# Optimization experiments

Measured on AMD Instinct MI355X. Metric: run time of the kernel, lower is better.

## Reference

```python
import jax, jax.numpy as jnp
import numpy as np

N_ATOMS = 25000
N_PAIRS = 500000
N_PROP = 16
C = 64          # channel width of pp/pi/ii/out layers
N_BASIS = 4     # radial basis functions per pair
DEPTH = 4       # number of GC blocks


def setup_inputs() -> dict:
    key = jax.random.key(0)
    ks = jax.random.split(key, 16)

    def w(k, shape):
        fan_in = shape[-2]
        return jax.random.normal(k, shape, jnp.float32) / jnp.sqrt(jnp.float32(fan_in))

    return {
        "ind_2": jax.random.randint(ks[0], (N_PAIRS, 2), 0, N_ATOMS),
        "prop": jax.random.normal(ks[1], (N_ATOMS, N_PROP), jnp.float32),
        "basis": jax.random.uniform(ks[2], (N_PAIRS, N_BASIS), jnp.float32),
        "pp0_w1": w(ks[3], (N_PROP, C)),
        "pp0_b1": jnp.zeros((C,), jnp.float32),
        "pp_w1": w(ks[4], (DEPTH - 1, C, C)),
        "pp_b1": jnp.zeros((DEPTH - 1, C), jnp.float32),
        "pp_w2": w(ks[5], (DEPTH, C, C)),
        "pp_b2": jnp.zeros((DEPTH, C), jnp.float32),
        "pi_w1": w(ks[6], (DEPTH, 2 * C, C)),
        "pi_b1": jnp.zeros((DEPTH, C), jnp.float32),
        "pi_w2": w(ks[7], (DEPTH, C, C * N_BASIS)),
        "pi_b2": jnp.zeros((DEPTH, C * N_BASIS), jnp.float32),
        "ii_w1": w(ks[8], (DEPTH, C, C)),
        "ii_w2": w(ks[9], (DEPTH, C, C)),
        "res0_w": w(ks[10], (N_PROP, C)),
        "out_w1": w(ks[11], (DEPTH, C, C)),
        "out_b1": jnp.zeros((DEPTH, C), jnp.float32),
        "out_w2": w(ks[12], (DEPTH, C, C)),
        "out_b2": jnp.zeros((DEPTH, C), jnp.float32),
        "out_wo": w(ks[13], (DEPTH, C, 1)),
    }


def _pinet_forward(ind_2, prop, basis,
                   pp0_w1, pp0_b1, pp_w1, pp_b1, pp_w2, pp_b2,
                   pi_w1, pi_b1, pi_w2, pi_b2,
                   ii_w1, ii_w2, res0_w,
                   out_w1, out_b1, out_w2, out_b2, out_wo):
    act = jnp.tanh
    n_atoms = prop.shape[0]
    n_basis = basis.shape[-1]
    c = pi_w2.shape[-1] // n_basis  # pi output channels
    depth = pp_w2.shape[0]
    ind_i = ind_2[:, 0]
    ind_j = ind_2[:, 1]

    p = prop
    output = jnp.zeros((n_atoms, out_wo.shape[-1]), p.dtype)
    for d in range(depth):
        # PPLayer (FFLayer with bias)
        if d == 0:
            h = act(p @ pp0_w1 + pp0_b1)
        else:
            h = act(p @ pp_w1[d - 1] + pp_b1[d - 1])
        h = act(h @ pp_w2[d] + pp_b2[d])
        # PILayer: gather pair endpoints, concat, FFLayer, basis contraction
        pij = jnp.concatenate([h[ind_i], h[ind_j]], axis=-1)  # (P, 2C)
        ww = act(pij @ pi_w1[d] + pi_b1[d])                   # (P, C)
        ww = act(ww @ pi_w2[d] + pi_b2[d])                    # (P, C*B)
        ww = ww.reshape(-1, c, n_basis)                       # (P, C, B)
        inter = jnp.einsum('pcb,pb->pc', ww, basis)           # (P, C)
        # IILayer (FFLayer, no bias)
        inter = act(inter @ ii_w1[d])
        inter = act(inter @ ii_w2[d])
        # IPLayer: scatter-sum pairs back to atoms
        newp = jax.ops.segment_sum(inter, ind_i, num_segments=n_atoms)
        # ResUpdate: linear projection if dims differ (block 0), else plain sum
        p = (p @ res0_w + newp) if d == 0 else (p + newp)
        # OutLayer: FFLayer + biasless linear, accumulated over depth
        o = act(p @ out_w1[d] + out_b1[d])
        o = act(o @ out_w2[d] + out_b2[d])
        output = output + o @ out_wo[d]
    return output


def reference(ind_2, prop, basis,
              pp0_w1, pp0_b1, pp_w1, pp_b1, pp_w2, pp_b2,
              pi_w1, pi_b1, pi_w2, pi_b2,
              ii_w1, ii_w2, res0_w,
              out_w1, out_b1, out_w2, out_b2, out_wo):
    return _pinet_forward(ind_2, prop, basis,
                          pp0_w1, pp0_b1, pp_w1, pp_b1, pp_w2, pp_b2,
                          pi_w1, pi_b1, pi_w2, pi_b2,
                          ii_w1, ii_w2, res0_w,
                          out_w1, out_b1, out_w2, out_b2, out_wo)
```

## Files before the change

kernel.cpp:

```cpp
#include <hip/hip_runtime.h>
#include <hip/hip_bf16.h>

#define N_ATOMS 25000
#define N_PAIRS 500000
#define DEPTH 4

typedef _Float16 f16x8 __attribute__((ext_vector_type(8)));
typedef float f32x16 __attribute__((ext_vector_type(16)));
typedef unsigned short u16;

__device__ __forceinline__ float tanh_fast(float x) {
    float e = __expf(2.0f * x);
    return 1.0f - 2.0f * __builtin_amdgcn_rcpf(e + 1.0f);
}

__device__ __forceinline__ void split_h(float x, u16& hi, u16& lo) {
    _Float16 h = (_Float16)x;
    _Float16 l = (_Float16)(x - (float)h);
    hi = *(u16*)&h;
    lo = *(u16*)&l;
}

__device__ __forceinline__ int swz8(int u) { return u ^ ((u >> 5) & 7); }

__global__ __launch_bounds__(256)
void prep_kernel(const float* __restrict__ piW1, const float* __restrict__ piW2,
                 const float* __restrict__ iiW1, const float* __restrict__ iiW2,
                 u16* __restrict__ img1, u16* __restrict__ img2, u16* __restrict__ imgab) {
    int gid = blockIdx.x * 256 + threadIdx.x;
    int d = gid >> 15, e = gid & 32767;
    u16 hi, lo;
    if (e < 8192) {
        int k = e >> 6, n = e & 63;
        split_h(piW1[d * 8192 + e], hi, lo);
        int ntw = n >> 5, colb = n & 31;
        int ks = k >> 4, lh = (k >> 3) & 1, j = k & 7;
        int off = ((ntw * 8 + ks) * 64 + lh * 32 + colb) * 8 + j;
        img1[d * 16384 + 0 * 8192 + off] = hi;
        img1[d * 16384 + 1 * 8192 + off] = lo;
    } else if (e < 24576) {
        int s = e - 8192;
        int k = s >> 8, n = s & 255;
        split_h(piW2[d * 16384 + s], hi, lo);
        int ch = n >> 2, t = n & 3;
        int ntw = ch >> 5, colb = ch & 31;
        int ks = k >> 4, lh = (k >> 3) & 1, j = k & 7;
        int off = (((ntw * 4 + t) * 4 + ks) * 64 + lh * 32 + colb) * 8 + j;
        img2[d * 32768 + 0 * 16384 + off] = hi;
        img2[d * 32768 + 1 * 16384 + off] = lo;
    } else {
        int stage = (e < 28672) ? 0 : 1;
        int s = e - (stage ? 28672 : 24576);
        int k = s >> 6, n = s & 63;
        float x = stage ? iiW2[d * 4096 + s] : iiW1[d * 4096 + s];
        split_h(x, hi, lo);
        int ntw = n >> 5, colb = n & 31;
        int ks = k >> 4, lh = (k >> 3) & 1, j = k & 7;
        int off = ((ntw * 4 + ks) * 64 + lh * 32 + colb) * 8 + j;
        imgab[d * 16384 + (stage * 2 + 0) * 4096 + off] = hi;
        imgab[d * 16384 + (stage * 2 + 1) * 4096 + off] = lo;
    }
}

__global__ __launch_bounds__(256)
void prep_b2(const float* __restrict__ piB2, float* __restrict__ b2p) {
    int d = blockIdx.x, n = threadIdx.x;
    int ch = n >> 2, t = n & 3;
    int np = (ch >> 5) * 128 + t * 32 + (ch & 31);
    b2p[d * 256 + np] = piB2[d * 256 + n];
}

template <int K, bool IS_D0>
__global__ __launch_bounds__(256)
void atom_mlp(const float* __restrict__ p_in,
              const float* __restrict__ W1, const float* __restrict__ b1,
              const float* __restrict__ W2, const float* __restrict__ b2,
              const float* __restrict__ res0_w,
              _Float16* __restrict__ h_hi, _Float16* __restrict__ h_lo,
              float* __restrict__ acc_out) {
    __shared__ float sP[4][64];
    __shared__ float sH[4][64];
    int tid = threadIdx.x;
    int al = tid >> 6, c = tid & 63;
    int a = blockIdx.x * 4 + al;
    if (c < K) sP[al][c] = p_in[a * K + c];
    __syncthreads();
    float s = b1[c];
#pragma unroll
    for (int k = 0; k < K; ++k) s += sP[al][k] * W1[k * 64 + c];
    float t1 = tanh_fast(s);
    float r;
    if (IS_D0) {
        r = 0.f;
#pragma unroll
        for (int k = 0; k < 16; ++k) r += sP[al][k] * res0_w[k * 64 + c];
    } else {
        r = sP[al][c];
    }
    acc_out[a * 64 + c] = r;
    sH[al][c] = t1;
    __syncthreads();
    float s2 = b2[c];
#pragma unroll
    for (int k = 0; k < 64; ++k) s2 += sH[al][k] * W2[k * 64 + c];
    float hv = tanh_fast(s2);
    _Float16 hb = (_Float16)hv;
    h_hi[a * 64 + c] = hb;
    h_lo[a * 64 + c] = (_Float16)(hv - (float)hb);
}

__global__ __launch_bounds__(256)
void out_kernel(const float* __restrict__ p,
                const float* __restrict__ W1, const float* __restrict__ b1,
                const float* __restrict__ W2, const float* __restrict__ b2,
                const float* __restrict__ wo,
                float* __restrict__ out, int store) {
    __shared__ float sP[4][64];
    __shared__ float sH[4][64];
    int tid = threadIdx.x;
    int al = tid >> 6, c = tid & 63;
    int a = blockIdx.x * 4 + al;
    sP[al][c] = p[a * 64 + c];
    __syncthreads();
    float s = b1[c];
#pragma unroll
    for (int k = 0; k < 64; ++k) s += sP[al][k] * W1[k * 64 + c];
    sH[al][c] = tanh_fast(s);
    __syncthreads();
    float s2 = b2[c];
#pragma unroll
    for (int k = 0; k < 64; ++k) s2 += sH[al][k] * W2[k * 64 + c];
    float v = tanh_fast(s2) * wo[c];
#pragma unroll
    for (int off = 32; off > 0; off >>= 1) v += __shfl_down(v, off, 64);
    if (c == 0) {
        if (store) out[a] = v;
        else out[a] += v;
    }
}

#define MFMA __builtin_amdgcn_mfma_f32_32x32x16_f16

__global__ __launch_bounds__(512, 2)
void pair_kernel(const _Float16* __restrict__ hhi,
                 const _Float16* __restrict__ hlo,
                 const int* __restrict__ ind2,
                 const float* __restrict__ basis,
                 const u16* __restrict__ img1,
                 const u16* __restrict__ img2,
                 const u16* __restrict__ imgab,
                 const float* __restrict__ piB1,
                 const float* __restrict__ b2p,
                 float* __restrict__ accp) {
    __shared__ __attribute__((aligned(16))) _Float16 sW2[32768];
    __shared__ __attribute__((aligned(16))) _Float16 sW1lo[8192];
    __shared__ __attribute__((aligned(16))) _Float16 sA[16384];
    __shared__ __attribute__((aligned(16))) _Float16 sAlo[8192];
    __shared__ __attribute__((aligned(16))) _Float16 sPing[8192];
    __shared__ float sBas[128 * 4];
    __shared__ int sIdx[128];

    const int tid = threadIdx.x;
    for (int i = tid; i < 4096; i += 512) ((uint4*)sW2)[i] = ((const uint4*)img2)[i];
    for (int i = tid; i < 1024; i += 512) ((uint4*)sW1lo)[i] = ((const uint4*)(img1 + 8192))[i];

    const int l = tid & 63;
    const int w = tid >> 6;
    const int mt = w >> 1, ntw = w & 1;
    const int col = l & 31, kg = l >> 5;
    const int ch = ntw * 32 + col;
    const int chks = ch >> 4, chlh = (ch >> 3) & 1, chj = ch & 7;

    int rb[4], wb[4];
    {
        const int wxor = 2 * chks + chlh;
#pragma unroll
        for (int c = 0; c < 4; ++c) {
            rb[c] = (l ^ (kg + 2 * c)) << 4;
            wb[c] = (mt * 4 + chks) * 1024 + chlh * 512 + ((((c) + 4 * kg) ^ wxor) << 4) + chj * 2;
        }
    }
    const int mtsA = mt << 13;
    const int mts  = mt << 12;

    f16x8 w1h[8], fa[2][4], fb[2][4];
#pragma unroll
    for (int ks = 0; ks < 8; ++ks)
        w1h[ks] = *(const f16x8*)(img1 + ntw * 4096 + ks * 512 + l * 8);
#pragma unroll
    for (int hl = 0; hl < 2; ++hl)
#pragma unroll
        for (int ks = 0; ks < 4; ++ks) {
            fa[hl][ks] = *(const f16x8*)(imgab + (0 * 2 + hl) * 4096 + ntw * 2048 + ks * 512 + l * 8);
            fb[hl][ks] = *(const f16x8*)(imgab + (1 * 2 + hl) * 4096 + ntw * 2048 + ks * 512 + l * 8);
        }
    const float b1v = piB1[ch];
    float b2v[4];
#pragma unroll
    for (int t = 0; t < 4; ++t) b2v[t] = b2p[ntw * 128 + t * 32 + col];

    const int nTiles = (N_PAIRS + 127) >> 7;

    auto gather = [&](int tile) {
        int base = tile << 7;
#pragma unroll
        for (int it = 0; it < 6; ++it) {
            int id = it * 512 + tid;
            if (id < 2048) {
                int m = id >> 4, half = (id >> 3) & 1, seg = id & 7;
                int p = base + m;
                uint4 v = make_uint4(0u, 0u, 0u, 0u);
                if (p < N_PAIRS) {
                    int row = ind2[2 * p + half];
                    v = *(const uint4*)(hhi + row * 64 + seg * 8);
                }
                int mtd = m >> 5, lrow = m & 31;
                int ks = half * 4 + (seg >> 1), lh = seg & 1;
                int u = (mtd * 8 + ks) * 64 + lh * 32 + lrow;
                *(uint4*)(sA + swz8(u) * 8) = v;
            } else {
                int e = id - 2048;
                int m = e >> 3, seg = e & 7;
                int p = base + m;
                uint4 v = make_uint4(0u, 0u, 0u, 0u);
                if (p < N_PAIRS) {
                    int row = ind2[2 * p];
                    v = *(const uint4*)(hlo + row * 64 + seg * 8);
                }
                int mtd = m >> 5, lrow = m & 31;
                int ks = seg >> 1, lh = seg & 1;
                int u = (mtd * 4 + ks) * 64 + lh * 32 + lrow;
                *(uint4*)(sAlo + swz8(u) * 8) = v;
            }
        }
    };
    gather(blockIdx.x);
    __syncthreads();

    for (int tile = blockIdx.x; tile < nTiles; tile += gridDim.x) {
        const int base = tile << 7;

        if (tid < 128) {
            int p = base + tid;
            float4 bv = (p < N_PAIRS) ? ((const float4*)basis)[p] : make_float4(0.f, 0.f, 0.f, 0.f);
            *(float4*)&sBas[tid * 4] = bv;
            sIdx[tid] = (p < N_PAIRS) ? ind2[2 * p] : 0;
        }
        {
            f32x16 acc = {};
            const char* blo = (const char*)(sW1lo + ntw * 4096 + l * 8);
#pragma unroll
            for (int ks = 0; ks < 8; ++ks) {
                f16x8 a = *(const f16x8*)((const char*)sA + mtsA + ks * 1024 + rb[ks & 3]);
                acc = MFMA(a, w1h[ks], acc, 0, 0, 0);
                acc = MFMA(a, *(const f16x8*)(blo + ks * 1024), acc, 0, 0, 0);
            }
#pragma unroll
            for (int ks = 0; ks < 4; ++ks) {
                f16x8 a = *(const f16x8*)((const char*)sAlo + mts + ks * 1024 + rb[ks]);
                acc = MFMA(a, w1h[ks], acc, 0, 0, 0);
            }
#pragma unroll
            for (int r = 0; r < 16; ++r)
                *(u16*)((char*)sPing + wb[r & 3] + ((r >> 2) << 7)) =
                    __builtin_bit_cast(u16, (_Float16)tanh_fast(acc[r] + b1v));
        }
        __syncthreads();

        {
            f32x16 acc[4] = {{}, {}, {}, {}};
#pragma unroll
            for (int ks = 0; ks < 4; ++ks) {
                f16x8 a = *(const f16x8*)((const char*)sPing + mts + ks * 1024 + rb[ks]);
#pragma unroll
                for (int t = 0; t < 4; ++t) {
                    acc[t] = MFMA(a, *(const f16x8*)(sW2 + ((ntw * 4 + t) * 4 + ks) * 512 + l * 8), acc[t], 0, 0, 0);
                    acc[t] = MFMA(a, *(const f16x8*)(sW2 + 16384 + ((ntw * 4 + t) * 4 + ks) * 512 + l * 8), acc[t], 0, 0, 0);
                }
            }
#pragma unroll
            for (int r = 0; r < 16; ++r) {
                int lrow = (r & 3) + 8 * (r >> 2) + 4 * kg;
                int row = mt * 32 + lrow;
                float4 bas = *(const float4*)&sBas[row * 4];
                float s = tanh_fast(acc[0][r] + b2v[0]) * bas.x
                        + tanh_fast(acc[1][r] + b2v[1]) * bas.y
                        + tanh_fast(acc[2][r] + b2v[2]) * bas.z
                        + tanh_fast(acc[3][r] + b2v[3]) * bas.w;
                *(u16*)((char*)sA + wb[r & 3] + ((r >> 2) << 7)) =
                    __builtin_bit_cast(u16, (_Float16)s);
            }
        }
        __syncthreads();

        {
            f32x16 acc = {};
#pragma unroll
            for (int ks = 0; ks < 4; ++ks) {
                f16x8 a = *(const f16x8*)((const char*)sA + mts + ks * 1024 + rb[ks]);
                acc = MFMA(a, fa[0][ks], acc, 0, 0, 0);
                acc = MFMA(a, fa[1][ks], acc, 0, 0, 0);
            }
#pragma unroll
            for (int r = 0; r < 16; ++r)
                *(u16*)((char*)sPing + wb[r & 3] + ((r >> 2) << 7)) =
                    __builtin_bit_cast(u16, (_Float16)tanh_fast(acc[r]));
        }
        __syncthreads();

        {
            f16x8 afr[4];
#pragma unroll
            for (int ks = 0; ks < 4; ++ks)
                afr[ks] = *(const f16x8*)((const char*)sPing + mts + ks * 1024 + rb[ks]);

            gather(tile + gridDim.x);

            f32x16 acc = {};
#pragma unroll
            for (int ks = 0; ks < 4; ++ks) {
                acc = MFMA(afr[ks], fb[0][ks], acc, 0, 0, 0);
                acc = MFMA(afr[ks], fb[1][ks], acc, 0, 0, 0);
            }
#pragma unroll
            for (int r = 0; r < 16; ++r) {
                int lrow = (r & 3) + 8 * (r >> 2) + 4 * kg;
                int p = base + mt * 32 + lrow;
                if (p < N_PAIRS)
                    atomicAdd(&accp[sIdx[mt * 32 + lrow] * 64 + ch], tanh_fast(acc[r]));
            }
        }
        __syncthreads();
    }
}

extern "C" void kernel_launch(void* const* d_in, const int* in_sizes, int n_in,
                              void* d_out, int out_size, void* d_ws, size_t ws_size,
                              hipStream_t stream) {
    const int* ind2 = (const int*)d_in[0];
    const float* prop = (const float*)d_in[1];
    const float* basis = (const float*)d_in[2];
    const float* pp0_w1 = (const float*)d_in[3];
    const float* pp0_b1 = (const float*)d_in[4];
    const float* pp_w1 = (const float*)d_in[5];
    const float* pp_b1 = (const float*)d_in[6];
    const float* pp_w2 = (const float*)d_in[7];
    const float* pp_b2 = (const float*)d_in[8];
    const float* pi_w1 = (const float*)d_in[9];
    const float* pi_b1 = (const float*)d_in[10];
    const float* pi_w2 = (const float*)d_in[11];
    const float* pi_b2 = (const float*)d_in[12];
    const float* ii_w1 = (const float*)d_in[13];
    const float* ii_w2 = (const float*)d_in[14];
    const float* res0_w = (const float*)d_in[15];
    const float* out_w1 = (const float*)d_in[16];
    const float* out_b1 = (const float*)d_in[17];
    const float* out_w2 = (const float*)d_in[18];
    const float* out_b2 = (const float*)d_in[19];
    const float* out_wo = (const float*)d_in[20];
    float* out = (float*)d_out;

    float* B0 = (float*)d_ws;
    float* B1 = B0 + N_ATOMS * 64;
    _Float16* Hhi = (_Float16*)(B1 + N_ATOMS * 64);
    _Float16* Hlo = Hhi + N_ATOMS * 64;
    u16* img1 = (u16*)(Hlo + N_ATOMS * 64);
    u16* img2 = img1 + 4 * 16384;
    u16* imgab = img2 + 4 * 32768;
    float* b2p = (float*)(imgab + 4 * 16384);
    float* pbuf[2] = {B0, B1};

    prep_kernel<<<512, 256, 0, stream>>>(pi_w1, pi_w2, ii_w1, ii_w2, img1, img2, imgab);
    prep_b2<<<4, 256, 0, stream>>>(pi_b2, b2p);

    for (int d = 0; d < DEPTH; ++d) {
        float* acc = pbuf[d & 1];
        if (d == 0) {
            atom_mlp<16, true><<<N_ATOMS / 4, 256, 0, stream>>>(
                prop, pp0_w1, pp0_b1, pp_w2, pp_b2, res0_w, Hhi, Hlo, acc);
        } else {
            const float* pin = pbuf[(d - 1) & 1];
            atom_mlp<64, false><<<N_ATOMS / 4, 256, 0, stream>>>(
                pin, pp_w1 + (d - 1) * 4096, pp_b1 + (d - 1) * 64,
                pp_w2 + d * 4096, pp_b2 + d * 64, nullptr, Hhi, Hlo, acc);
        }
        pair_kernel<<<256, 512, 0, stream>>>(
            Hhi, Hlo, ind2, basis,
            img1 + d * 16384, img2 + d * 32768, imgab + d * 16384,
            pi_b1 + d * 64, b2p + d * 256, acc);
        out_kernel<<<N_ATOMS / 4, 256, 0, stream>>>(
            acc, out_w1 + d * 4096, out_b1 + d * 64,
            out_w2 + d * 4096, out_b2 + d * 64, out_wo + d * 64,
            out, d == 0 ? 1 : 0);
    }
}
```

Measured before the change: 1.048 ms.

## Fuse out-layer with next atom MLP and double-buffer pair metadata

Merges the per-depth output MLP with the next block's atom MLP into one kernel that reads the atom state once, writes the copy used as the next accumulator, and emits the hi/lo fp16 split. This removes three kernel launches and repeated reads of the atom state. The basis and index loads for the next tile move into the prefetch gather with double-buffered shared arrays. The block-wide barriers become an LDS-only wait plus s_barrier, so outstanding global loads from the prefetch no longer stall each barrier. The LDS-only wait is correct only as long as no global results are consumed across those barriers before they arrive.

After: 1.043 ms. About the same (-0.5%).

```diff
diff --git a/kernel.cpp b/kernel.cpp
--- a/kernel.cpp
+++ b/kernel.cpp
@@ -19,6 +19,11 @@
     _Float16 l = (_Float16)(x - (float)h);
     hi = *(u16*)&h;
     lo = *(u16*)&l;
+}
+
+__device__ __forceinline__ void bar_lgkm() {
+    asm volatile("s_waitcnt lgkmcnt(0)" ::: "memory");
+    __builtin_amdgcn_s_barrier();
 }
 
 __device__ __forceinline__ int swz8(int u) { return u ^ ((u >> 5) & 7); }
@@ -139,6 +144,55 @@
     }
 }
 
+__global__ __launch_bounds__(256)
+void fused_out_atom(const float* __restrict__ p,
+                    const float* __restrict__ oW1, const float* __restrict__ ob1,
+                    const float* __restrict__ oW2, const float* __restrict__ ob2,
+                    const float* __restrict__ wo,
+                    const float* __restrict__ aW1, const float* __restrict__ ab1,
+                    const float* __restrict__ aW2, const float* __restrict__ ab2,
+                    float* __restrict__ out, int store,
+                    _Float16* __restrict__ h_hi, _Float16* __restrict__ h_lo,
+                    float* __restrict__ acc_out) {
+    __shared__ float sP[4][64];
+    __shared__ float sHo[4][64];
+    __shared__ float sHa[4][64];
+    int tid = threadIdx.x;
+    int al = tid >> 6, c = tid & 63;
+    int a = blockIdx.x * 4 + al;
+    float pv = p[a * 64 + c];
+    sP[al][c] = pv;
+    acc_out[a * 64 + c] = pv;
+    __syncthreads();
+    float so = ob1[c], sa = ab1[c];
+#pragma unroll
+    for (int k = 0; k < 64; ++k) {
+        float x = sP[al][k];
+        so += x * oW1[k * 64 + c];
+        sa += x * aW1[k * 64 + c];
+    }
+    sHo[al][c] = tanh_fast(so);
+    sHa[al][c] = tanh_fast(sa);
+    __syncthreads();
+    float s2o = ob2[c], s2a = ab2[c];
+#pragma unroll
+    for (int k = 0; k < 64; ++k) {
+        s2o += sHo[al][k] * oW2[k * 64 + c];
+        s2a += sHa[al][k] * aW2[k * 64 + c];
+    }
+    float v = tanh_fast(s2o) * wo[c];
+#pragma unroll
+    for (int off = 32; off > 0; off >>= 1) v += __shfl_down(v, off, 64);
+    if (c == 0) {
+        if (store) out[a] = v;
+        else out[a] += v;
+    }
+    float hv = tanh_fast(s2a);
+    _Float16 hb = (_Float16)hv;
+    h_hi[a * 64 + c] = hb;
+    h_lo[a * 64 + c] = (_Float16)(hv - (float)hb);
+}
+
 #define MFMA __builtin_amdgcn_mfma_f32_32x32x16_f16
 
 __global__ __launch_bounds__(512, 2)
@@ -157,8 +211,8 @@
     __shared__ __attribute__((aligned(16))) _Float16 sA[16384];
     __shared__ __attribute__((aligned(16))) _Float16 sAlo[8192];
     __shared__ __attribute__((aligned(16))) _Float16 sPing[8192];
-    __shared__ float sBas[128 * 4];
-    __shared__ int sIdx[128];
+    __shared__ float sBas[2][128 * 4];
+    __shared__ int sIdx[2][128];
 
     const int tid = threadIdx.x;
     for (int i = tid; i < 4096; i += 512) ((uint4*)sW2)[i] = ((const uint4*)img2)[i];
@@ -201,8 +255,14 @@
 
     const int nTiles = (N_PAIRS + 127) >> 7;
 
-    auto gather = [&](int tile) {
+    auto gather = [&](int tile, int pb) {
         int base = tile << 7;
+        if (tid < 128) {
+            int p = base + tid;
+            float4 bv = (p < N_PAIRS) ? ((const float4*)basis)[p] : make_float4(0.f, 0.f, 0.f, 0.f);
+            *(float4*)&sBas[pb][tid * 4] = bv;
+            sIdx[pb][tid] = (p < N_PAIRS) ? ind2[2 * p] : 0;
+        }
 #pragma unroll
         for (int it = 0; it < 6; ++it) {
             int id = it * 512 + tid;
@@ -234,18 +294,13 @@
             }
         }
     };
-    gather(blockIdx.x);
-    __syncthreads();
-
+    gather(blockIdx.x, 0);
+    __syncthreads();
+
+    int pb = 0;
     for (int tile = blockIdx.x; tile < nTiles; tile += gridDim.x) {
         const int base = tile << 7;
 
-        if (tid < 128) {
-            int p = base + tid;
-            float4 bv = (p < N_PAIRS) ? ((const float4*)basis)[p] : make_float4(0.f, 0.f, 0.f, 0.f);
-            *(float4*)&sBas[tid * 4] = bv;
-            sIdx[tid] = (p < N_PAIRS) ? ind2[2 * p] : 0;
-        }
         {
             f32x16 acc = {};
             const char* blo = (const char*)(sW1lo + ntw * 4096 + l * 8);
@@ -265,7 +320,7 @@
                 *(u16*)((char*)sPing + wb[r & 3] + ((r >> 2) << 7)) =
                     __builtin_bit_cast(u16, (_Float16)tanh_fast(acc[r] + b1v));
         }
-        __syncthreads();
+        bar_lgkm();
 
         {
             f32x16 acc[4] = {{}, {}, {}, {}};
@@ -282,7 +337,7 @@
             for (int r = 0; r < 16; ++r) {
                 int lrow = (r & 3) + 8 * (r >> 2) + 4 * kg;
                 int row = mt * 32 + lrow;
-                float4 bas = *(const float4*)&sBas[row * 4];
+                float4 bas = *(const float4*)&sBas[pb][row * 4];
                 float s = tanh_fast(acc[0][r] + b2v[0]) * bas.x
                         + tanh_fast(acc[1][r] + b2v[1]) * bas.y
                         + tanh_fast(acc[2][r] + b2v[2]) * bas.z
@@ -291,7 +346,7 @@
                     __builtin_bit_cast(u16, (_Float16)s);
             }
         }
-        __syncthreads();
+        bar_lgkm();
 
         {
             f32x16 acc = {};
@@ -306,7 +361,7 @@
                 *(u16*)((char*)sPing + wb[r & 3] + ((r >> 2) << 7)) =
                     __builtin_bit_cast(u16, (_Float16)tanh_fast(acc[r]));
         }
-        __syncthreads();
+        bar_lgkm();
 
         {
             f16x8 afr[4];
@@ -314,7 +369,7 @@
             for (int ks = 0; ks < 4; ++ks)
                 afr[ks] = *(const f16x8*)((const char*)sPing + mts + ks * 1024 + rb[ks]);
 
-            gather(tile + gridDim.x);
+            gather(tile + gridDim.x, pb ^ 1);
 
             f32x16 acc = {};
 #pragma unroll
@@ -327,10 +382,11 @@
                 int lrow = (r & 3) + 8 * (r >> 2) + 4 * kg;
                 int p = base + mt * 32 + lrow;
                 if (p < N_PAIRS)
-                    atomicAdd(&accp[sIdx[mt * 32 + lrow] * 64 + ch], tanh_fast(acc[r]));
-            }
-        }
-        __syncthreads();
+                    atomicAdd(&accp[sIdx[pb][mt * 32 + lrow] * 64 + ch], tanh_fast(acc[r]));
+            }
+        }
+        bar_lgkm();
+        pb ^= 1;
     }
 }
 
@@ -380,17 +436,22 @@
                 prop, pp0_w1, pp0_b1, pp_w2, pp_b2, res0_w, Hhi, Hlo, acc);
         } else {
             const float* pin = pbuf[(d - 1) & 1];
-            atom_mlp<64, false><<<N_ATOMS / 4, 256, 0, stream>>>(
-                pin, pp_w1 + (d - 1) * 4096, pp_b1 + (d - 1) * 64,
-                pp_w2 + d * 4096, pp_b2 + d * 64, nullptr, Hhi, Hlo, acc);
+            fused_out_atom<<<N_ATOMS / 4, 256, 0, stream>>>(
+                pin,
+                out_w1 + (d - 1) * 4096, out_b1 + (d - 1) * 64,
+                out_w2 + (d - 1) * 4096, out_b2 + (d - 1) * 64, out_wo + (d - 1) * 64,
+                pp_w1 + (d - 1) * 4096, pp_b1 + (d - 1) * 64,
+                pp_w2 + d * 4096, pp_b2 + d * 64,
+                out, (d - 1) == 0 ? 1 : 0,
+                Hhi, Hlo, acc);
         }
         pair_kernel<<<256, 512, 0, stream>>>(
             Hhi, Hlo, ind2, basis,
             img1 + d * 16384, img2 + d * 32768, imgab + d * 16384,
             pi_b1 + d * 64, b2p + d * 256, acc);
-        out_kernel<<<N_ATOMS / 4, 256, 0, stream>>>(
-            acc, out_w1 + d * 4096, out_b1 + d * 64,
-            out_w2 + d * 4096, out_b2 + d * 64, out_wo + d * 64,
-            out, d == 0 ? 1 : 0);
-    }
-}
+    }
+    out_kernel<<<N_ATOMS / 4, 256, 0, stream>>>(
+        pbuf[(DEPTH - 1) & 1], out_w1 + (DEPTH - 1) * 4096, out_b1 + (DEPTH - 1) * 64,
+        out_w2 + (DEPTH - 1) * 4096, out_b2 + (DEPTH - 1) * 64, out_wo + (DEPTH - 1) * 64,
+        out, 0);
+}
```
